# Optimization experiments

Hardware: AMD Instinct MI355X
Metric: run time of the kernel (lower is better)

## Reference

```python
import jax, jax.numpy as jnp
import numpy as np

HIDDEN = 512
TEMPERATURE = float(np.sqrt(HIDDEN))  # scaled-dot temperature
BATCH = 64


def _build_weights(attn_weight, N, K):
    """Vectorized version of get_attn_weight: (S,S,H) with S = N*K+1.
    Regions: 0=same_sample, 1=same_class, 2=diff_class, 3=support->query,
    4=query->support, 5=query->query. Replicates the torch overwrite order."""
    S = N * K + 1
    NK = N * K
    i = jnp.arange(S)[:, None]
    j = jnp.arange(S)[None, :]
    idx = jnp.full((S, S), 2, dtype=jnp.int32)                      # w_diff_class
    idx = jnp.where((i // K) == (j // K), 1, idx)                   # w_same_class
    idx = jnp.where((i < NK) & (j == NK), 3, idx)                   # w_stoquery
    idx = jnp.where(i == j, 0, idx)                                 # w_same_sample (diag)
    idx = jnp.where((i == NK) & (j < NK), 4, idx)                   # w_querytos
    idx = jnp.where((i == NK) & (j == NK), 5, idx)                  # w_query
    return attn_weight[idx]  # (S, S, H)


def setup_inputs() -> dict:
    key = jax.random.key(0)
    kq, kk, kv, kw = jax.random.split(key, 4)
    N, K = 10, 10
    S = N * K + 1  # 101
    q = jax.random.normal(kq, (BATCH, S, HIDDEN), dtype=jnp.float32)
    k = jax.random.normal(kk, (BATCH, S, HIDDEN), dtype=jnp.float32)
    v = jax.random.normal(kv, (BATCH, S, HIDDEN), dtype=jnp.float32)
    bound = float(np.sqrt(6 / 2))
    attn_weight = jax.random.uniform(kw, (6, HIDDEN), dtype=jnp.float32,
                                     minval=-bound, maxval=bound)
    return {"q": q, "k": k, "v": v, "attn_weight": attn_weight, "N": N, "K": K}


def reference(q, k, v, attn_weight, N, K):
    # attn[b,i,j] = softmax_j(q.k^T / temperature)
    scores = jnp.einsum("bih,bjh->bij", q, k) / TEMPERATURE
    attn = jax.nn.softmax(scores, axis=2)  # dropout p=0 (eval) -> identity
    weights = _build_weights(attn_weight, N, K)  # (S,S,H)
    # out[b,i,h] = sum_j attn[b,i,j] * weights[i,j,h] * v[b,j,h]
    out = jnp.einsum("bij,ijh,bjh->bih", attn, weights, v)
    return out, attn
```

## Files before the change

kernel.cpp:

```cpp
#include <hip/hip_runtime.h>
#include <math.h>
#include <stdint.h>

#define BATCH 64
#define SEQ   101
#define HID   512
#define NKQ   100
#define KCLS  10
#define INV_TEMP 0.04419417382415922f
#define SPAD  128

typedef short bf16x8 __attribute__((ext_vector_type(8)));
typedef float f32x4  __attribute__((ext_vector_type(4)));

__device__ inline void split_bf16(float x, short& hi, short& lo) {
    uint32_t u = __builtin_bit_cast(uint32_t, x);
    hi = (short)(u >> 16);
    float hf = __builtin_bit_cast(float, u & 0xFFFF0000u);
    float l  = x - hf;
    lo = (short)(__builtin_bit_cast(uint32_t, l) >> 16);
}

__global__ __launch_bounds__(256)
void fused_attn(const float* __restrict__ q, const float* __restrict__ k,
                const float* __restrict__ v, const float* __restrict__ aw,
                float* __restrict__ out, float* __restrict__ attn) {
    __shared__ float sc[32][132];
    __shared__ short ah_s[32][136];
    __shared__ short al_s[32][136];
    __shared__ short mh_s[32][136];
    __shared__ short ml_s[32][136];

    const int b   = blockIdx.y;
    const int i0  = blockIdx.x * 32;
    const int tid = threadIdx.x;
    const int wv  = tid >> 6, lane = tid & 63;
    const int m   = lane & 15;
    const int kq  = (lane >> 4) * 8;
    const int col = lane & 15, rq = (lane >> 4) * 4;

    const float* qb = q + (size_t)b * SEQ * HID;
    const float* kb = k + (size_t)b * SEQ * HID;
    const float* vb = v + (size_t)b * SEQ * HID;

    {
        const int j0w = wv * 32;
        f32x4 acc[2][2] = {};
        for (int ks = 0; ks < HID; ks += 32) {
            bf16x8 qh[2], ql[2], kh[2], kl[2];
            #pragma unroll
            for (int it = 0; it < 2; ++it) {
                const int row = i0 + it * 16 + m;
                float x[8];
                if (row < SEQ) {
                    float4 u0 = *(const float4*)(qb + (size_t)row * HID + ks + kq);
                    float4 u1 = *(const float4*)(qb + (size_t)row * HID + ks + kq + 4);
                    x[0]=u0.x; x[1]=u0.y; x[2]=u0.z; x[3]=u0.w;
                    x[4]=u1.x; x[5]=u1.y; x[6]=u1.z; x[7]=u1.w;
                } else {
                    #pragma unroll
                    for (int e = 0; e < 8; ++e) x[e] = 0.f;
                }
                #pragma unroll
                for (int e = 0; e < 8; ++e) { short h,l; split_bf16(x[e],h,l); qh[it][e]=h; ql[it][e]=l; }
            }
            #pragma unroll
            for (int jt = 0; jt < 2; ++jt) {
                const int row = j0w + jt * 16 + m;
                float x[8];
                if (row < SEQ) {
                    float4 u0 = *(const float4*)(kb + (size_t)row * HID + ks + kq);
                    float4 u1 = *(const float4*)(kb + (size_t)row * HID + ks + kq + 4);
                    x[0]=u0.x; x[1]=u0.y; x[2]=u0.z; x[3]=u0.w;
                    x[4]=u1.x; x[5]=u1.y; x[6]=u1.z; x[7]=u1.w;
                } else {
                    #pragma unroll
                    for (int e = 0; e < 8; ++e) x[e] = 0.f;
                }
                #pragma unroll
                for (int e = 0; e < 8; ++e) { short h,l; split_bf16(x[e],h,l); kh[jt][e]=h; kl[jt][e]=l; }
            }
            #pragma unroll
            for (int it = 0; it < 2; ++it)
                #pragma unroll
                for (int jt = 0; jt < 2; ++jt) {
                    acc[it][jt] = __builtin_amdgcn_mfma_f32_16x16x32_bf16(qh[it], kh[jt], acc[it][jt], 0, 0, 0);
                    acc[it][jt] = __builtin_amdgcn_mfma_f32_16x16x32_bf16(qh[it], kl[jt], acc[it][jt], 0, 0, 0);
                    acc[it][jt] = __builtin_amdgcn_mfma_f32_16x16x32_bf16(ql[it], kh[jt], acc[it][jt], 0, 0, 0);
                }
        }
        #pragma unroll
        for (int it = 0; it < 2; ++it)
            #pragma unroll
            for (int jt = 0; jt < 2; ++jt)
                #pragma unroll
                for (int r = 0; r < 4; ++r)
                    sc[it * 16 + rq + r][j0w + jt * 16 + col] = acc[it][jt][r];
    }
    __syncthreads();

    {
        const int row = tid >> 3, t8 = tid & 7;
        const int gi  = i0 + row;
        float mx = -1e30f;
        for (int j = t8; j < SEQ; j += 8) {
            float s = sc[row][j] * INV_TEMP;
            sc[row][j] = s;
            mx = fmaxf(mx, s);
        }
        #pragma unroll
        for (int off = 1; off < 8; off <<= 1) mx = fmaxf(mx, __shfl_xor(mx, off));
        float sum = 0.f;
        for (int j = t8; j < SEQ; j += 8) {
            float e = __expf(sc[row][j] - mx);
            sc[row][j] = e;
            sum += e;
        }
        #pragma unroll
        for (int off = 1; off < 8; off <<= 1) sum += __shfl_xor(sum, off);
        const float inv = 1.f / sum;
        const int ci = gi / KCLS;
        float* arow = attn + ((size_t)b * SEQ + gi) * SEQ;
        for (int j = t8; j < SEQ; j += 8) {
            float a = sc[row][j] * inv;
            sc[row][j] = a;
            if (gi < SEQ) arow[j] = a;
            short h, l; split_bf16(a, h, l);
            ah_s[row][j] = h; al_s[row][j] = l;
            bool msk = (j / KCLS) == ci;
            mh_s[row][j] = msk ? h : (short)0;
            ml_s[row][j] = msk ? l : (short)0;
        }
        for (int j = SEQ + t8; j < 136; j += 8) {
            ah_s[row][j] = 0; al_s[row][j] = 0;
            mh_s[row][j] = 0; ml_s[row][j] = 0;
        }
    }
    __syncthreads();

    const int hw = wv * 128;
    #pragma unroll
    for (int half = 0; half < 2; ++half) {
        f32x4 T[2][4] = {}, U[2][4] = {};
        #pragma unroll
        for (int ks = 0; ks < SPAD; ks += 32) {
            bf16x8 Ah[2], Al[2], Mh[2], Ml[2];
            #pragma unroll
            for (int it = 0; it < 2; ++it) {
                const int il = it * 16 + m;
                Ah[it] = *(const bf16x8*)&ah_s[il][ks + kq];
                Al[it] = *(const bf16x8*)&al_s[il][ks + kq];
                Mh[it] = *(const bf16x8*)&mh_s[il][ks + kq];
                Ml[it] = *(const bf16x8*)&ml_s[il][ks + kq];
            }
            #pragma unroll
            for (int ht4 = 0; ht4 < 4; ++ht4) {
                const int h = hw + (half * 4 + ht4) * 16 + m;
                float x[8];
                #pragma unroll
                for (int e = 0; e < 8; ++e) {
                    const int j = ks + kq + e;
                    x[e] = (j < SEQ) ? vb[(size_t)j * HID + h] : 0.f;
                }
                bf16x8 Bh, Bl;
                #pragma unroll
                for (int e = 0; e < 8; ++e) { short hh,ll; split_bf16(x[e],hh,ll); Bh[e]=hh; Bl[e]=ll; }
                #pragma unroll
                for (int it = 0; it < 2; ++it) {
                    T[it][ht4] = __builtin_amdgcn_mfma_f32_16x16x32_bf16(Ah[it], Bh, T[it][ht4], 0, 0, 0);
                    T[it][ht4] = __builtin_amdgcn_mfma_f32_16x16x32_bf16(Ah[it], Bl, T[it][ht4], 0, 0, 0);
                    T[it][ht4] = __builtin_amdgcn_mfma_f32_16x16x32_bf16(Al[it], Bh, T[it][ht4], 0, 0, 0);
                    U[it][ht4] = __builtin_amdgcn_mfma_f32_16x16x32_bf16(Mh[it], Bh, U[it][ht4], 0, 0, 0);
                    U[it][ht4] = __builtin_amdgcn_mfma_f32_16x16x32_bf16(Mh[it], Bl, U[it][ht4], 0, 0, 0);
                    U[it][ht4] = __builtin_amdgcn_mfma_f32_16x16x32_bf16(Ml[it], Bh, U[it][ht4], 0, 0, 0);
                }
            }
        }
        #pragma unroll
        for (int ht4 = 0; ht4 < 4; ++ht4) {
            const int h = hw + (half * 4 + ht4) * 16 + col;
            const float w0 = aw[0 * HID + h], w1 = aw[1 * HID + h], w2 = aw[2 * HID + h];
            const float w3 = aw[3 * HID + h], w4 = aw[4 * HID + h], w5 = aw[5 * HID + h];
            const float vN = vb[(size_t)NKQ * HID + h];
            #pragma unroll
            for (int it = 0; it < 2; ++it)
                #pragma unroll
                for (int r = 0; r < 4; ++r) {
                    const int il = it * 16 + rq + r;
                    const int i  = i0 + il;
                    if (i >= SEQ) continue;
                    const float t = T[it][ht4][r], u = U[it][ht4][r];
                    const float aiN = sc[il][NKQ];
                    float o;
                    if (i < NKQ) {
                        const float aii = sc[il][i];
                        const float vi  = vb[(size_t)i * HID + h];
                        o = w2 * t + (w1 - w2) * u + (w0 - w1) * aii * vi + (w3 - w2) * aiN * vN;
                    } else {
                        o = w4 * t + (w5 - w4) * aiN * vN;
                    }
                    out[((size_t)b * SEQ + i) * HID + h] = o;
                }
        }
    }
}

extern "C" void kernel_launch(void* const* d_in, const int* in_sizes, int n_in,
                              void* d_out, int out_size, void* d_ws, size_t ws_size,
                              hipStream_t stream) {
    const float* q  = (const float*)d_in[0];
    const float* k  = (const float*)d_in[1];
    const float* v  = (const float*)d_in[2];
    const float* aw = (const float*)d_in[3];
    float* out  = (float*)d_out;
    float* attn = out + (size_t)BATCH * SEQ * HID;

    fused_attn<<<dim3(4, BATCH), dim3(256), 0, stream>>>(q, k, v, aw, out, attn);
}
```

Before: 133.9 us.

## Shrink row tile to 16 with 8 waves and drop masked low-part MFMAs

Moves from 4 row-blocks of 32 rows with 4 waves to 7 blocks of 16 rows with 8 waves, giving 448 workgroups instead of 256 so more of the GPU is occupied. Each wave now computes one 16x16 score tile and a 64-wide slice of hidden in the PV stage. The same-class masked product keeps only the hi*hi bf16 term, dropping two MFMAs and the ml_s buffer. The tradeoffs are lower accuracy in U, V being re-read by more blocks, and fewer output rows per wave.

```diff
diff --git a/kernel.cpp b/kernel.cpp
--- a/kernel.cpp
+++ b/kernel.cpp
@@ -21,186 +21,150 @@
     lo = (short)(__builtin_bit_cast(uint32_t, l) >> 16);
 }
 
-__global__ __launch_bounds__(256)
+__global__ __launch_bounds__(512, 4)
 void fused_attn(const float* __restrict__ q, const float* __restrict__ k,
                 const float* __restrict__ v, const float* __restrict__ aw,
                 float* __restrict__ out, float* __restrict__ attn) {
-    __shared__ float sc[32][132];
-    __shared__ short ah_s[32][136];
-    __shared__ short al_s[32][136];
-    __shared__ short mh_s[32][136];
-    __shared__ short ml_s[32][136];
+    __shared__ float sc[16][132];
+    __shared__ short ah_s[16][136];
+    __shared__ short al_s[16][136];
+    __shared__ short mh_s[16][136];
 
     const int b   = blockIdx.y;
-    const int i0  = blockIdx.x * 32;
+    const int i0  = blockIdx.x * 16;
     const int tid = threadIdx.x;
     const int wv  = tid >> 6, lane = tid & 63;
     const int m   = lane & 15;
     const int kq  = (lane >> 4) * 8;
-    const int col = lane & 15, rq = (lane >> 4) * 4;
+    const int rq  = (lane >> 4) * 4;
 
     const float* qb = q + (size_t)b * SEQ * HID;
     const float* kb = k + (size_t)b * SEQ * HID;
     const float* vb = v + (size_t)b * SEQ * HID;
 
     {
-        const int j0w = wv * 32;
-        f32x4 acc[2][2] = {};
+        const int j0w = wv * 16;
+        const int qrow = i0 + m;
+        const int krow = j0w + m;
+        f32x4 acc = {};
         for (int ks = 0; ks < HID; ks += 32) {
-            bf16x8 qh[2], ql[2], kh[2], kl[2];
-            #pragma unroll
-            for (int it = 0; it < 2; ++it) {
-                const int row = i0 + it * 16 + m;
-                float x[8];
-                if (row < SEQ) {
-                    float4 u0 = *(const float4*)(qb + (size_t)row * HID + ks + kq);
-                    float4 u1 = *(const float4*)(qb + (size_t)row * HID + ks + kq + 4);
-                    x[0]=u0.x; x[1]=u0.y; x[2]=u0.z; x[3]=u0.w;
-                    x[4]=u1.x; x[5]=u1.y; x[6]=u1.z; x[7]=u1.w;
-                } else {
-                    #pragma unroll
-                    for (int e = 0; e < 8; ++e) x[e] = 0.f;
-                }
+            float x[8];
+            bf16x8 qh, ql, kh, kl;
+            if (qrow < SEQ) {
+                float4 u0 = *(const float4*)(qb + (size_t)qrow * HID + ks + kq);
+                float4 u1 = *(const float4*)(qb + (size_t)qrow * HID + ks + kq + 4);
+                x[0]=u0.x; x[1]=u0.y; x[2]=u0.z; x[3]=u0.w;
+                x[4]=u1.x; x[5]=u1.y; x[6]=u1.z; x[7]=u1.w;
+            } else {
                 #pragma unroll
-                for (int e = 0; e < 8; ++e) { short h,l; split_bf16(x[e],h,l); qh[it][e]=h; ql[it][e]=l; }
+                for (int e = 0; e < 8; ++e) x[e] = 0.f;
             }
             #pragma unroll
-            for (int jt = 0; jt < 2; ++jt) {
-                const int row = j0w + jt * 16 + m;
-                float x[8];
-                if (row < SEQ) {
-                    float4 u0 = *(const float4*)(kb + (size_t)row * HID + ks + kq);
-                    float4 u1 = *(const float4*)(kb + (size_t)row * HID + ks + kq + 4);
-                    x[0]=u0.x; x[1]=u0.y; x[2]=u0.z; x[3]=u0.w;
-                    x[4]=u1.x; x[5]=u1.y; x[6]=u1.z; x[7]=u1.w;
-                } else {
-                    #pragma unroll
-                    for (int e = 0; e < 8; ++e) x[e] = 0.f;
-                }
+            for (int e = 0; e < 8; ++e) { short h,l; split_bf16(x[e],h,l); qh[e]=h; ql[e]=l; }
+            if (krow < SEQ) {
+                float4 u0 = *(const float4*)(kb + (size_t)krow * HID + ks + kq);
+                float4 u1 = *(const float4*)(kb + (size_t)krow * HID + ks + kq + 4);
+                x[0]=u0.x; x[1]=u0.y; x[2]=u0.z; x[3]=u0.w;
+                x[4]=u1.x; x[5]=u1.y; x[6]=u1.z; x[7]=u1.w;
+            } else {
                 #pragma unroll
-                for (int e = 0; e < 8; ++e) { short h,l; split_bf16(x[e],h,l); kh[jt][e]=h; kl[jt][e]=l; }
+                for (int e = 0; e < 8; ++e) x[e] = 0.f;
             }
             #pragma unroll
-            for (int it = 0; it < 2; ++it)
-                #pragma unroll
-                for (int jt = 0; jt < 2; ++jt) {
-                    acc[it][jt] = __builtin_amdgcn_mfma_f32_16x16x32_bf16(qh[it], kh[jt], acc[it][jt], 0, 0, 0);
-                    acc[it][jt] = __builtin_amdgcn_mfma_f32_16x16x32_bf16(qh[it], kl[jt], acc[it][jt], 0, 0, 0);
-                    acc[it][jt] = __builtin_amdgcn_mfma_f32_16x16x32_bf16(ql[it], kh[jt], acc[it][jt], 0, 0, 0);
-                }
+            for (int e = 0; e < 8; ++e) { short h,l; split_bf16(x[e],h,l); kh[e]=h; kl[e]=l; }
+            acc = __builtin_amdgcn_mfma_f32_16x16x32_bf16(qh, kh, acc, 0, 0, 0);
+            acc = __builtin_amdgcn_mfma_f32_16x16x32_bf16(qh, kl, acc, 0, 0, 0);
+            acc = __builtin_amdgcn_mfma_f32_16x16x32_bf16(ql, kh, acc, 0, 0, 0);
         }
         #pragma unroll
-        for (int it = 0; it < 2; ++it)
-            #pragma unroll
-            for (int jt = 0; jt < 2; ++jt)
-                #pragma unroll
-                for (int r = 0; r < 4; ++r)
-                    sc[it * 16 + rq + r][j0w + jt * 16 + col] = acc[it][jt][r];
+        for (int r = 0; r < 4; ++r)
+            sc[rq + r][j0w + m] = acc[r];
     }
     __syncthreads();
 
     {
-        const int row = tid >> 3, t8 = tid & 7;
+        const int row = tid >> 5, t32 = tid & 31;
         const int gi  = i0 + row;
         float mx = -1e30f;
-        for (int j = t8; j < SEQ; j += 8) {
+        for (int j = t32; j < SEQ; j += 32) {
             float s = sc[row][j] * INV_TEMP;
             sc[row][j] = s;
             mx = fmaxf(mx, s);
         }
         #pragma unroll
-        for (int off = 1; off < 8; off <<= 1) mx = fmaxf(mx, __shfl_xor(mx, off));
+        for (int off = 1; off < 32; off <<= 1) mx = fmaxf(mx, __shfl_xor(mx, off));
         float sum = 0.f;
-        for (int j = t8; j < SEQ; j += 8) {
+        for (int j = t32; j < SEQ; j += 32) {
             float e = __expf(sc[row][j] - mx);
             sc[row][j] = e;
             sum += e;
         }
         #pragma unroll
-        for (int off = 1; off < 8; off <<= 1) sum += __shfl_xor(sum, off);
+        for (int off = 1; off < 32; off <<= 1) sum += __shfl_xor(sum, off);
         const float inv = 1.f / sum;
         const int ci = gi / KCLS;
         float* arow = attn + ((size_t)b * SEQ + gi) * SEQ;
-        for (int j = t8; j < SEQ; j += 8) {
+        for (int j = t32; j < SEQ; j += 32) {
             float a = sc[row][j] * inv;
             sc[row][j] = a;
             if (gi < SEQ) arow[j] = a;
             short h, l; split_bf16(a, h, l);
             ah_s[row][j] = h; al_s[row][j] = l;
-            bool msk = (j / KCLS) == ci;
-            mh_s[row][j] = msk ? h : (short)0;
-            ml_s[row][j] = msk ? l : (short)0;
+            mh_s[row][j] = ((j / KCLS) == ci) ? h : (short)0;
         }
-        for (int j = SEQ + t8; j < 136; j += 8) {
-            ah_s[row][j] = 0; al_s[row][j] = 0;
-            mh_s[row][j] = 0; ml_s[row][j] = 0;
+        for (int j = SEQ + t32; j < 136; j += 32) {
+            ah_s[row][j] = 0; al_s[row][j] = 0; mh_s[row][j] = 0;
         }
     }
     __syncthreads();
 
-    const int hw = wv * 128;
+    const int hw = wv * 64;
+    f32x4 T[4] = {}, U[4] = {};
+    for (int ks = 0; ks < SPAD; ks += 32) {
+        const bf16x8 Ah = *(const bf16x8*)&ah_s[m][ks + kq];
+        const bf16x8 Al = *(const bf16x8*)&al_s[m][ks + kq];
+        const bf16x8 Mh = *(const bf16x8*)&mh_s[m][ks + kq];
+        #pragma unroll
+        for (int ht = 0; ht < 4; ++ht) {
+            const int h = hw + ht * 16 + m;
+            float x[8];
+            #pragma unroll
+            for (int e = 0; e < 8; ++e) {
+                const int j = ks + kq + e;
+                x[e] = (j < SEQ) ? vb[(size_t)j * HID + h] : 0.f;
+            }
+            bf16x8 Bh, Bl;
+            #pragma unroll
+            for (int e = 0; e < 8; ++e) { short hh,ll; split_bf16(x[e],hh,ll); Bh[e]=hh; Bl[e]=ll; }
+            T[ht] = __builtin_amdgcn_mfma_f32_16x16x32_bf16(Ah, Bh, T[ht], 0, 0, 0);
+            T[ht] = __builtin_amdgcn_mfma_f32_16x16x32_bf16(Ah, Bl, T[ht], 0, 0, 0);
+            T[ht] = __builtin_amdgcn_mfma_f32_16x16x32_bf16(Al, Bh, T[ht], 0, 0, 0);
+            U[ht] = __builtin_amdgcn_mfma_f32_16x16x32_bf16(Mh, Bh, U[ht], 0, 0, 0);
+        }
+    }
+
     #pragma unroll
-    for (int half = 0; half < 2; ++half) {
-        f32x4 T[2][4] = {}, U[2][4] = {};
+    for (int ht = 0; ht < 4; ++ht) {
+        const int h = hw + ht * 16 + m;
+        const float w0 = aw[0 * HID + h], w1 = aw[1 * HID + h], w2 = aw[2 * HID + h];
+        const float w3 = aw[3 * HID + h], w4 = aw[4 * HID + h], w5 = aw[5 * HID + h];
+        const float vN = vb[(size_t)NKQ * HID + h];
         #pragma unroll
-        for (int ks = 0; ks < SPAD; ks += 32) {
-            bf16x8 Ah[2], Al[2], Mh[2], Ml[2];
-            #pragma unroll
-            for (int it = 0; it < 2; ++it) {
-                const int il = it * 16 + m;
-                Ah[it] = *(const bf16x8*)&ah_s[il][ks + kq];
-                Al[it] = *(const bf16x8*)&al_s[il][ks + kq];
-                Mh[it] = *(const bf16x8*)&mh_s[il][ks + kq];
-                Ml[it] = *(const bf16x8*)&ml_s[il][ks + kq];
+        for (int r = 0; r < 4; ++r) {
+            const int il = rq + r;
+            const int i  = i0 + il;
+            if (i >= SEQ) continue;
+            const float t = T[ht][r], u = U[ht][r];
+            const float aiN = sc[il][NKQ];
+            float o;
+            if (i < NKQ) {
+                const float aii = sc[il][i];
+                const float vi  = vb[(size_t)i * HID + h];
+                o = w2 * t + (w1 - w2) * u + (w0 - w1) * aii * vi + (w3 - w2) * aiN * vN;
+            } else {
+                o = w4 * t + (w5 - w4) * aiN * vN;
             }
-            #pragma unroll
-            for (int ht4 = 0; ht4 < 4; ++ht4) {
-                const int h = hw + (half * 4 + ht4) * 16 + m;
-                float x[8];
-                #pragma unroll
-                for (int e = 0; e < 8; ++e) {
-                    const int j = ks + kq + e;
-                    x[e] = (j < SEQ) ? vb[(size_t)j * HID + h] : 0.f;
-                }
-                bf16x8 Bh, Bl;
-                #pragma unroll
-                for (int e = 0; e < 8; ++e) { short hh,ll; split_bf16(x[e],hh,ll); Bh[e]=hh; Bl[e]=ll; }
-                #pragma unroll
-                for (int it = 0; it < 2; ++it) {
-                    T[it][ht4] = __builtin_amdgcn_mfma_f32_16x16x32_bf16(Ah[it], Bh, T[it][ht4], 0, 0, 0);
-                    T[it][ht4] = __builtin_amdgcn_mfma_f32_16x16x32_bf16(Ah[it], Bl, T[it][ht4], 0, 0, 0);
-                    T[it][ht4] = __builtin_amdgcn_mfma_f32_16x16x32_bf16(Al[it], Bh, T[it][ht4], 0, 0, 0);
-                    U[it][ht4] = __builtin_amdgcn_mfma_f32_16x16x32_bf16(Mh[it], Bh, U[it][ht4], 0, 0, 0);
-                    U[it][ht4] = __builtin_amdgcn_mfma_f32_16x16x32_bf16(Mh[it], Bl, U[it][ht4], 0, 0, 0);
-                    U[it][ht4] = __builtin_amdgcn_mfma_f32_16x16x32_bf16(Ml[it], Bh, U[it][ht4], 0, 0, 0);
-                }
-            }
-        }
-        #pragma unroll
-        for (int ht4 = 0; ht4 < 4; ++ht4) {
-            const int h = hw + (half * 4 + ht4) * 16 + col;
-            const float w0 = aw[0 * HID + h], w1 = aw[1 * HID + h], w2 = aw[2 * HID + h];
-            const float w3 = aw[3 * HID + h], w4 = aw[4 * HID + h], w5 = aw[5 * HID + h];
-            const float vN = vb[(size_t)NKQ * HID + h];
-            #pragma unroll
-            for (int it = 0; it < 2; ++it)
-                #pragma unroll
-                for (int r = 0; r < 4; ++r) {
-                    const int il = it * 16 + rq + r;
-                    const int i  = i0 + il;
-                    if (i >= SEQ) continue;
-                    const float t = T[it][ht4][r], u = U[it][ht4][r];
-                    const float aiN = sc[il][NKQ];
-                    float o;
-                    if (i < NKQ) {
-                        const float aii = sc[il][i];
-                        const float vi  = vb[(size_t)i * HID + h];
-                        o = w2 * t + (w1 - w2) * u + (w0 - w1) * aii * vi + (w3 - w2) * aiN * vN;
-                    } else {
-                        o = w4 * t + (w5 - w4) * aiN * vN;
-                    }
-                    out[((size_t)b * SEQ + i) * HID + h] = o;
-                }
+            out[((size_t)b * SEQ + i) * HID + h] = o;
         }
     }
 }
@@ -215,5 +179,5 @@
     float* out  = (float*)d_out;
     float* attn = out + (size_t)BATCH * SEQ * HID;
 
-    fused_attn<<<dim3(4, BATCH), dim3(256), 0, stream>>>(q, k, v, aw, out, attn);
+    fused_attn<<<dim3(7, BATCH), dim3(512), 0, stream>>>(q, k, v, aw, out, attn);
 }
```

New measurement: 127.3 us. -4.9%, faster.
